# Kernel optimization log

Measured on AMD Instinct MI355X. Metric: run time of the kernel, lower is better.

## Reference

```python
import jax, jax.numpy as jnp
import numpy as np

D = 768
B = 32
N = 768


def setup_inputs() -> dict:
    key = jax.random.key(0)
    k1, k2, k3, k4 = jax.random.split(key, 4)
    stdv = 1.0 / np.sqrt(D)
    X = jax.random.normal(k1, (B, N, D), dtype=jnp.float32)
    adj = jax.random.uniform(k2, (B, N, N), dtype=jnp.float32)
    W_l = jax.random.uniform(k3, (D, D), dtype=jnp.float32, minval=-stdv, maxval=stdv)
    W_l1 = jax.random.uniform(k4, (D, D), dtype=jnp.float32, minval=-stdv, maxval=stdv)
    return {"X": X, "adj": adj, "W_l": W_l, "W_l1": W_l1}


def _row_normalize(adj):
    # rowsum^-1 with inf -> 0 (rows summing to zero stay zero)
    rowsum = adj.sum(axis=-1, keepdims=True)  # [B, N, 1]
    r_inv = jnp.where(rowsum == 0, 0.0, 1.0 / rowsum)
    return adj * r_inv


def reference(X, adj, W_l, W_l1):
    # X: [B, N, D], adj: [B, N, N]
    adj_n = _row_normalize(adj)
    e1 = jnp.einsum('bnd,de->bne', X, W_l1)        # message transform
    e11 = jnp.einsum('bnm,bmd->bnd', adj_n, e1)    # aggregate
    X1 = jnp.einsum('bnd,de->bne', X, W_l)         # self transform
    h = X1 + e11
    return jax.nn.leaky_relu(h, negative_slope=0.01)
```

## Files before the change

### kernel.cpp

```cpp
#include <hip/hip_runtime.h>
#include <hip/hip_bf16.h>
#include <cstdint>
#include <cstddef>

#define BN_ROWS 24576
#define DD 768
#define BE (768*768)
#define BM 192
#define BN_T 192
#define BK 32
#define ABUF 12288
#define BUFSZ 24576

typedef __attribute__((ext_vector_type(8))) short bf16x8;
typedef __attribute__((ext_vector_type(4))) float f32x4;
typedef __attribute__((ext_vector_type(8))) unsigned short u16x8;

static __device__ __forceinline__ unsigned short f2bf(float f) {
  unsigned int u = __builtin_bit_cast(unsigned int, f);
  unsigned int lsb = (u >> 16) & 1u;
  u += 0x7fffu + lsb;
  return (unsigned short)(u >> 16);
}

static __device__ __forceinline__ u16x8 pack8(float4 a, float4 b) {
  u16x8 o;
  o[0] = f2bf(a.x); o[1] = f2bf(a.y); o[2] = f2bf(a.z); o[3] = f2bf(a.w);
  o[4] = f2bf(b.x); o[5] = f2bf(b.y); o[6] = f2bf(b.z); o[7] = f2bf(b.w);
  return o;
}

#define CXB 2304
#define CXS (CXB * 256)

__global__ __launch_bounds__(256) void convertX(const float* __restrict__ x,
                                                unsigned short* __restrict__ xb) {
  const int u0 = blockIdx.x * 256 + threadIdx.x;
  const float4* in = reinterpret_cast<const float4*>(x);
  u16x8* outp = reinterpret_cast<u16x8*>(xb);
  float4 v[8];
  #pragma unroll
  for (int j = 0; j < 4; ++j) {
    v[2 * j]     = in[(size_t)(u0 + j * CXS) * 2];
    v[2 * j + 1] = in[(size_t)(u0 + j * CXS) * 2 + 1];
  }
  #pragma unroll
  for (int j = 0; j < 4; ++j)
    outp[u0 + j * CXS] = pack8(v[2 * j], v[2 * j + 1]);
}

#define ANB 3072

__global__ __launch_bounds__(256) void prep2(const float* __restrict__ adj,
                                             const float* __restrict__ Wl,
                                             const float* __restrict__ Wl1,
                                             unsigned short* __restrict__ adjnb,
                                             unsigned short* __restrict__ WlT,
                                             unsigned short* __restrict__ Wl1T) {
  __shared__ float tile[64][65];
  const int bid = blockIdx.x;
  if (bid < ANB) {
    const int w = threadIdx.x >> 6;
    const int hl = (threadIdx.x >> 5) & 1;
    const int l = threadIdx.x & 31;
    const int row = bid * 8 + w * 2 + hl;
    const float4* a = reinterpret_cast<const float4*>(adj + (size_t)row * DD);
    float4 v[6];
    #pragma unroll
    for (int i = 0; i < 3; ++i) {
      int u = l + i * 32;
      v[2 * i]     = a[u * 2];
      v[2 * i + 1] = a[u * 2 + 1];
    }
    float s = 0.f;
    #pragma unroll
    for (int i = 0; i < 6; ++i) s += (v[i].x + v[i].y) + (v[i].z + v[i].w);
    #pragma unroll
    for (int off = 16; off; off >>= 1) s += __shfl_xor(s, off);
    float rinv = (s == 0.f) ? 0.f : 1.f / s;
    u16x8* o = reinterpret_cast<u16x8*>(adjnb + (size_t)row * DD);
    #pragma unroll
    for (int i = 0; i < 3; ++i) {
      float4 p = v[2 * i], q = v[2 * i + 1];
      p.x *= rinv; p.y *= rinv; p.z *= rinv; p.w *= rinv;
      q.x *= rinv; q.y *= rinv; q.z *= rinv; q.w *= rinv;
      o[l + i * 32] = pack8(p, q);
    }
  } else {
    const int tb = bid - ANB;
    const int tr = tb / 12, tc = tb % 12;
    const int c = threadIdx.x & 63, r0 = threadIdx.x >> 6;
    const float* srcs[2] = {Wl, Wl1};
    unsigned short* dsts[2] = {WlT, Wl1T};
    #pragma unroll
    for (int m = 0; m < 2; ++m) {
      const float* src = srcs[m];
      #pragma unroll
      for (int i = 0; i < 16; ++i) {
        int r = r0 + i * 4;
        tile[r][c] = src[(size_t)(tr * 64 + r) * DD + tc * 64 + c];
      }
      __syncthreads();
      unsigned short* dst = dsts[m];
      #pragma unroll
      for (int i = 0; i < 16; ++i) {
        int r2 = r0 + i * 4;
        dst[(size_t)(tc * 64 + r2) * DD + tr * 64 + c] = f2bf(tile[c][r2]);
      }
      __syncthreads();
    }
  }
}


template<int MODE>
__global__ __launch_bounds__(256, 2) void gemm4(
    const unsigned short* __restrict__ P0,
    const unsigned short* __restrict__ P1,
    const unsigned short* __restrict__ P2,
    const unsigned short* __restrict__ P3,
    void* __restrict__ outp)
{
  __shared__ char smem[2 * BUFSZ];
  constexpr int NT = MODE ? 48 : 24;
  const int tid = threadIdx.x, lane = tid & 63;
  const int wid = tid >> 6;
  const int wr = wid >> 1, wc = wid & 1;

  const int logical = (blockIdx.x & 7) * 64 + (blockIdx.x >> 3);

  const unsigned short *Ab0, *Bb0, *Ab1 = nullptr, *Bb1 = nullptr;
  int mt, nt, b;
  if (MODE == 0) {
    mt = logical >> 2; nt = logical & 3;
    b = mt >> 2;
    Ab0 = P0 + (size_t)mt * BM * DD;
    Bb0 = P1 + (size_t)nt * BN_T * DD;
  } else {
    b = logical >> 4; int r = logical & 15; mt = r >> 2; nt = r & 3;
    size_t bo = (size_t)b * BE;
    Ab0 = P0 + bo + (size_t)mt * BM * DD;
    Bb0 = P1 + bo + (size_t)nt * BN_T * DD;
    Ab1 = P2 + bo + (size_t)mt * BM * DD;
    Bb1 = P3 + (size_t)nt * BN_T * DD;
  }

  const int r_in = lane >> 2;
  const int s_in = lane & 3;

  auto stage = [&](int s) {
    const int buf = (s & 1) * BUFSZ;
    const unsigned short *Ab, *Bb;
    int kk;
    if (MODE == 1 && s >= 24) { kk = s - 24; Ab = Ab1; Bb = Bb1; }
    else                      { kk = s;      Ab = Ab0; Bb = Bb0; }
    #pragma unroll
    for (int i = 0; i < 6; ++i) {
      int chunk = wid * 6 + i;
      bool isA = chunk < 12;
      int c = isA ? chunk : chunk - 12;
      int row = c * 16 + r_in;
      int slot = s_in ^ ((row >> 1) & 3);
      const unsigned short* src = (isA ? Ab : Bb) + (size_t)row * DD + kk * BK + slot * 8;
      __builtin_amdgcn_global_load_lds(
          (const __attribute__((address_space(1))) void*)src,
          (__attribute__((address_space(3))) void*)(smem + buf + (isA ? 0 : ABUF) + c * 1024),
          16, 0, 0);
    }
  };

  const int ks = lane >> 4;
  auto frag = [&](int off, int row) -> bf16x8 {
    int slot = ks ^ ((row >> 1) & 3);
    return *reinterpret_cast<const bf16x8*>(smem + off + row * 64 + slot * 16);
  };

  f32x4 acc[6][6] = {};
  const int arow = wr * 96 + (lane & 15);
  const int brow = wc * 96 + (lane & 15);

  stage(0);

  for (int t = 0; t < NT; ++t) {
    asm volatile("s_waitcnt vmcnt(0)" ::: "memory");
    __builtin_amdgcn_s_barrier();

    if (t + 1 < NT) stage(t + 1);

    const int bufA = (t & 1) * BUFSZ;
    const int bufB = bufA + ABUF;
    bf16x8 a[6], bg[6];
    #pragma unroll
    for (int i = 0; i < 6; ++i) a[i] = frag(bufA, arow + i * 16);
    #pragma unroll
    for (int i = 0; i < 6; ++i) bg[i] = frag(bufB, brow + i * 16);

    __builtin_amdgcn_s_setprio(1);
    #pragma unroll
    for (int ni = 0; ni < 6; ++ni)
      #pragma unroll
      for (int mi = 0; mi < 6; ++mi)
        acc[mi][ni] = __builtin_amdgcn_mfma_f32_16x16x32_bf16(a[mi], bg[ni], acc[mi][ni], 0, 0, 0);
    __builtin_amdgcn_s_setprio(0);
  }

  if (MODE == 0) {
    unsigned short* ob = (unsigned short*)outp + (size_t)b * BE;
    const int mloc = (mt & 3) * BM + wr * 96 + (lane >> 4) * 4;
    #pragma unroll
    for (int mi = 0; mi < 6; ++mi)
      #pragma unroll
      for (int ni = 0; ni < 6; ++ni) {
        int m = mloc + mi * 16;
        int d = nt * BN_T + wc * 96 + ni * 16 + (lane & 15);
        f32x4 v = acc[mi][ni];
        ushort4 o;
        o.x = f2bf(v[0]); o.y = f2bf(v[1]); o.z = f2bf(v[2]); o.w = f2bf(v[3]);
        *reinterpret_cast<ushort4*>(ob + (size_t)d * DD + m) = o;
      }
  } else {
    float* ob = (float*)outp + (size_t)b * BE;
    const int mloc = mt * BM + wr * 96 + (lane >> 4) * 4;
    #pragma unroll
    for (int mi = 0; mi < 6; ++mi)
      #pragma unroll
      for (int ni = 0; ni < 6; ++ni) {
        int m = mloc + mi * 16;
        int n = nt * BN_T + wc * 96 + ni * 16 + (lane & 15);
        f32x4 v = acc[mi][ni];
        #pragma unroll
        for (int j = 0; j < 4; ++j) {
          float x = v[j];
          ob[(size_t)(m + j) * DD + n] = x > 0.f ? x : 0.01f * x;
        }
      }
  }
}


extern "C" void kernel_launch(void* const* d_in, const int* in_sizes, int n_in,
                              void* d_out, int out_size, void* d_ws, size_t ws_size,
                              hipStream_t stream) {
  const float* X   = (const float*)d_in[0];
  const float* adj = (const float*)d_in[1];
  const float* Wl  = (const float*)d_in[2];
  const float* Wl1 = (const float*)d_in[3];
  float* out = (float*)d_out;

  char* ws = (char*)d_ws;
  const size_t SZ = (size_t)BN_ROWS * DD * 2;
  unsigned short* Xb    = (unsigned short*)(ws);
  unsigned short* adjnb = (unsigned short*)(ws + SZ);
  unsigned short* e1T   = (unsigned short*)(ws + 2 * SZ);
  unsigned short* WlT   = (unsigned short*)(ws + 3 * SZ);
  unsigned short* Wl1T  = (unsigned short*)(ws + 3 * SZ + (size_t)BE * 2);

  convertX<<<CXB, 256, 0, stream>>>(X, Xb);
  prep2<<<ANB + 144, 256, 0, stream>>>(adj, Wl, Wl1, adjnb, WlT, Wl1T);
  gemm4<0><<<512, 256, 0, stream>>>(Xb, Wl1T, nullptr, nullptr, e1T);
  gemm4<1><<<512, 256, 0, stream>>>(adjnb, e1T, Xb, WlT, out);
}
```

Measured before the change: 150.7 us.

## Switch GEMMs to 256x256 tiles with 8 waves and ping-pong quadrant pipelining

Replaces the 192x192, 4-wave GEMM with a 256x256, 8-wave (512-thread) kernel that uses BK=64 and a 128KB double-buffered LDS. The K step is split into four quadrant phases, and async loads of the next A/B halves are interleaved with MFMA work under fine-grained waitcnt and barriers. The grid shrinks to 288 blocks, one per CU. The aim is higher arithmetic intensity per LDS byte and better overlap of loads with MFMA, at the cost of many more barriers, heavy register pressure, and only one block per CU. 288 tiles on 256 CUs leaves a partial second wave.

```diff
diff --git a/kernel.cpp b/kernel.cpp
--- a/kernel.cpp
+++ b/kernel.cpp
@@ -6,11 +6,6 @@
 #define BN_ROWS 24576
 #define DD 768
 #define BE (768*768)
-#define BM 192
-#define BN_T 192
-#define BK 32
-#define ABUF 12288
-#define BUFSZ 24576
 
 typedef __attribute__((ext_vector_type(8))) short bf16x8;
 typedef __attribute__((ext_vector_type(4))) float f32x4;
@@ -114,105 +109,174 @@
 
 
 template<int MODE>
-__global__ __launch_bounds__(256, 2) void gemm4(
+__global__ __launch_bounds__(512) void gemm8p(
     const unsigned short* __restrict__ P0,
     const unsigned short* __restrict__ P1,
     const unsigned short* __restrict__ P2,
     const unsigned short* __restrict__ P3,
     void* __restrict__ outp)
 {
-  __shared__ char smem[2 * BUFSZ];
-  constexpr int NT = MODE ? 48 : 24;
+  __shared__ char smem[131072];
+  constexpr int NT = MODE ? 24 : 12;
   const int tid = threadIdx.x, lane = tid & 63;
   const int wid = tid >> 6;
-  const int wr = wid >> 1, wc = wid & 1;
-
-  const int logical = (blockIdx.x & 7) * 64 + (blockIdx.x >> 3);
-
-  const unsigned short *Ab0, *Bb0, *Ab1 = nullptr, *Bb1 = nullptr;
+  const int wr = wid >> 2, wc = wid & 3;
+
+  const int logical = (blockIdx.x & 7) * 36 + (blockIdx.x >> 3);
+
+  const unsigned short *Ag0, *Bg0, *Ag1 = nullptr, *Bg1 = nullptr;
   int mt, nt, b;
   if (MODE == 0) {
-    mt = logical >> 2; nt = logical & 3;
-    b = mt >> 2;
-    Ab0 = P0 + (size_t)mt * BM * DD;
-    Bb0 = P1 + (size_t)nt * BN_T * DD;
+    mt = logical / 3; nt = logical % 3;
+    b = mt / 3;
+    Ag0 = P0 + (size_t)mt * 256 * DD;
+    Bg0 = P1 + (size_t)nt * 256 * DD;
   } else {
-    b = logical >> 4; int r = logical & 15; mt = r >> 2; nt = r & 3;
+    b = logical / 9; int r = logical % 9; mt = r / 3; nt = r % 3;
     size_t bo = (size_t)b * BE;
-    Ab0 = P0 + bo + (size_t)mt * BM * DD;
-    Bb0 = P1 + bo + (size_t)nt * BN_T * DD;
-    Ab1 = P2 + bo + (size_t)mt * BM * DD;
-    Bb1 = P3 + (size_t)nt * BN_T * DD;
-  }
-
-  const int r_in = lane >> 2;
-  const int s_in = lane & 3;
-
-  auto stage = [&](int s) {
-    const int buf = (s & 1) * BUFSZ;
-    const unsigned short *Ab, *Bb;
-    int kk;
-    if (MODE == 1 && s >= 24) { kk = s - 24; Ab = Ab1; Bb = Bb1; }
-    else                      { kk = s;      Ab = Ab0; Bb = Bb0; }
-    #pragma unroll
-    for (int i = 0; i < 6; ++i) {
-      int chunk = wid * 6 + i;
-      bool isA = chunk < 12;
-      int c = isA ? chunk : chunk - 12;
-      int row = c * 16 + r_in;
-      int slot = s_in ^ ((row >> 1) & 3);
-      const unsigned short* src = (isA ? Ab : Bb) + (size_t)row * DD + kk * BK + slot * 8;
+    Ag0 = P0 + bo + (size_t)mt * 256 * DD;
+    Bg0 = P1 + bo + (size_t)nt * 256 * DD;
+    Ag1 = P2 + bo + (size_t)mt * 256 * DD;
+    Bg1 = P3 + (size_t)nt * 256 * DD;
+  }
+
+  const int srow_t = tid >> 3;
+  const int sslot = tid & 7;
+
+  auto stage = [&](int s, bool isA, int hi) {
+    int sc = s < NT ? s : 0;
+    int kk; const unsigned short* base;
+    if (MODE == 1 && sc >= 12) { kk = sc - 12; base = isA ? Ag1 : Bg1; }
+    else                       { kk = sc;      base = isA ? Ag0 : Bg0; }
+    char* region = smem + (s & 1) * 65536 + (isA ? 0 : 32768) + hi * 16384;
+    #pragma unroll
+    for (int l = 0; l < 2; ++l) {
+      int row = hi * 128 + l * 64 + srow_t;
+      const unsigned short* src = base + (size_t)row * DD + kk * 64
+                                  + (sslot ^ (row & 7)) * 8;
       __builtin_amdgcn_global_load_lds(
           (const __attribute__((address_space(1))) void*)src,
-          (__attribute__((address_space(3))) void*)(smem + buf + (isA ? 0 : ABUF) + c * 1024),
+          (__attribute__((address_space(3))) void*)(region + l * 8192 + wid * 1024),
           16, 0, 0);
     }
   };
 
   const int ks = lane >> 4;
-  auto frag = [&](int off, int row) -> bf16x8 {
-    int slot = ks ^ ((row >> 1) & 3);
-    return *reinterpret_cast<const bf16x8*>(smem + off + row * 64 + slot * 16);
+  const int l15 = lane & 15;
+  auto rdA = [&](int bufo, int rh, int fi, int kh) -> bf16x8 {
+    int row = wr * 128 + rh * 64 + fi * 16 + l15;
+    int slot = (kh * 4 + ks) ^ (row & 7);
+    return *reinterpret_cast<const bf16x8*>(smem + bufo + row * 128 + slot * 16);
   };
-
-  f32x4 acc[6][6] = {};
-  const int arow = wr * 96 + (lane & 15);
-  const int brow = wc * 96 + (lane & 15);
-
-  stage(0);
+  auto rdB = [&](int bufo, int ch, int fj, int kh) -> bf16x8 {
+    int row = wc * 64 + ch * 32 + fj * 16 + l15;
+    int slot = (kh * 4 + ks) ^ (row & 7);
+    return *reinterpret_cast<const bf16x8*>(smem + bufo + 32768 + row * 128 + slot * 16);
+  };
+
+  f32x4 acc[8][4] = {};
+  bf16x8 a0[8], a1[8], b0[4], b1[4];
+
+  stage(0, true, 0); stage(0, true, 1);
+  stage(0, false, 0); stage(0, false, 1);
+  stage(1, true, 0); stage(1, true, 1);
+  asm volatile("s_waitcnt vmcnt(4)" ::: "memory");
+  __builtin_amdgcn_s_barrier();
 
   for (int t = 0; t < NT; ++t) {
-    asm volatile("s_waitcnt vmcnt(0)" ::: "memory");
-    __builtin_amdgcn_s_barrier();
-
-    if (t + 1 < NT) stage(t + 1);
-
-    const int bufA = (t & 1) * BUFSZ;
-    const int bufB = bufA + ABUF;
-    bf16x8 a[6], bg[6];
-    #pragma unroll
-    for (int i = 0; i < 6; ++i) a[i] = frag(bufA, arow + i * 16);
-    #pragma unroll
-    for (int i = 0; i < 6; ++i) bg[i] = frag(bufB, brow + i * 16);
-
+    const int bufo = (t & 1) * 65536;
+
+    #pragma unroll
+    for (int fi = 0; fi < 4; ++fi) {
+      a0[fi * 2]     = rdA(bufo, 0, fi, 0);
+      a0[fi * 2 + 1] = rdA(bufo, 0, fi, 1);
+    }
+    #pragma unroll
+    for (int fj = 0; fj < 2; ++fj) {
+      b0[fj * 2]     = rdB(bufo, 0, fj, 0);
+      b0[fj * 2 + 1] = rdB(bufo, 0, fj, 1);
+    }
+    stage(t + 1, false, 0);
+    asm volatile("s_waitcnt vmcnt(4)" ::: "memory");
+    __builtin_amdgcn_s_barrier();
     __builtin_amdgcn_s_setprio(1);
     #pragma unroll
-    for (int ni = 0; ni < 6; ++ni)
-      #pragma unroll
-      for (int mi = 0; mi < 6; ++mi)
-        acc[mi][ni] = __builtin_amdgcn_mfma_f32_16x16x32_bf16(a[mi], bg[ni], acc[mi][ni], 0, 0, 0);
+    for (int kh = 0; kh < 2; ++kh)
+      #pragma unroll
+      for (int fi = 0; fi < 4; ++fi)
+        #pragma unroll
+        for (int fj = 0; fj < 2; ++fj)
+          acc[fi][fj] = __builtin_amdgcn_mfma_f32_16x16x32_bf16(
+              a0[fi * 2 + kh], b0[fj * 2 + kh], acc[fi][fj], 0, 0, 0);
     __builtin_amdgcn_s_setprio(0);
-  }
+    __builtin_amdgcn_s_barrier();
+
+    #pragma unroll
+    for (int fi = 0; fi < 4; ++fi) {
+      a1[fi * 2]     = rdA(bufo, 1, fi, 0);
+      a1[fi * 2 + 1] = rdA(bufo, 1, fi, 1);
+    }
+    stage(t + 1, false, 1);
+    asm volatile("s_waitcnt vmcnt(4)" ::: "memory");
+    __builtin_amdgcn_s_barrier();
+    __builtin_amdgcn_s_setprio(1);
+    #pragma unroll
+    for (int kh = 0; kh < 2; ++kh)
+      #pragma unroll
+      for (int fi = 0; fi < 4; ++fi)
+        #pragma unroll
+        for (int fj = 0; fj < 2; ++fj)
+          acc[4 + fi][fj] = __builtin_amdgcn_mfma_f32_16x16x32_bf16(
+              a1[fi * 2 + kh], b0[fj * 2 + kh], acc[4 + fi][fj], 0, 0, 0);
+    __builtin_amdgcn_s_setprio(0);
+    __builtin_amdgcn_s_barrier();
+
+    #pragma unroll
+    for (int fj = 0; fj < 2; ++fj) {
+      b1[fj * 2]     = rdB(bufo, 1, fj, 0);
+      b1[fj * 2 + 1] = rdB(bufo, 1, fj, 1);
+    }
+    stage(t + 2, true, 0);
+    asm volatile("s_waitcnt vmcnt(4)" ::: "memory");
+    __builtin_amdgcn_s_barrier();
+    __builtin_amdgcn_s_setprio(1);
+    #pragma unroll
+    for (int kh = 0; kh < 2; ++kh)
+      #pragma unroll
+      for (int fi = 0; fi < 4; ++fi)
+        #pragma unroll
+        for (int fj = 0; fj < 2; ++fj)
+          acc[4 + fi][2 + fj] = __builtin_amdgcn_mfma_f32_16x16x32_bf16(
+              a1[fi * 2 + kh], b1[fj * 2 + kh], acc[4 + fi][2 + fj], 0, 0, 0);
+    __builtin_amdgcn_s_setprio(0);
+    __builtin_amdgcn_s_barrier();
+
+    stage(t + 2, true, 1);
+    asm volatile("s_waitcnt vmcnt(4)" ::: "memory");
+    __builtin_amdgcn_s_barrier();
+    __builtin_amdgcn_s_setprio(1);
+    #pragma unroll
+    for (int kh = 0; kh < 2; ++kh)
+      #pragma unroll
+      for (int fi = 0; fi < 4; ++fi)
+        #pragma unroll
+        for (int fj = 0; fj < 2; ++fj)
+          acc[fi][2 + fj] = __builtin_amdgcn_mfma_f32_16x16x32_bf16(
+              a0[fi * 2 + kh], b1[fj * 2 + kh], acc[fi][2 + fj], 0, 0, 0);
+    __builtin_amdgcn_s_setprio(0);
+    __builtin_amdgcn_s_barrier();
+  }
+  asm volatile("s_waitcnt vmcnt(0)" ::: "memory");
 
   if (MODE == 0) {
     unsigned short* ob = (unsigned short*)outp + (size_t)b * BE;
-    const int mloc = (mt & 3) * BM + wr * 96 + (lane >> 4) * 4;
-    #pragma unroll
-    for (int mi = 0; mi < 6; ++mi)
-      #pragma unroll
-      for (int ni = 0; ni < 6; ++ni) {
+    const int mloc = (mt % 3) * 256 + wr * 128 + (lane >> 4) * 4;
+    #pragma unroll
+    for (int mi = 0; mi < 8; ++mi)
+      #pragma unroll
+      for (int ni = 0; ni < 4; ++ni) {
         int m = mloc + mi * 16;
-        int d = nt * BN_T + wc * 96 + ni * 16 + (lane & 15);
+        int d = nt * 256 + wc * 64 + ni * 16 + l15;
         f32x4 v = acc[mi][ni];
         ushort4 o;
         o.x = f2bf(v[0]); o.y = f2bf(v[1]); o.z = f2bf(v[2]); o.w = f2bf(v[3]);
@@ -220,13 +284,13 @@
       }
   } else {
     float* ob = (float*)outp + (size_t)b * BE;
-    const int mloc = mt * BM + wr * 96 + (lane >> 4) * 4;
-    #pragma unroll
-    for (int mi = 0; mi < 6; ++mi)
-      #pragma unroll
-      for (int ni = 0; ni < 6; ++ni) {
+    const int mloc = mt * 256 + wr * 128 + (lane >> 4) * 4;
+    #pragma unroll
+    for (int mi = 0; mi < 8; ++mi)
+      #pragma unroll
+      for (int ni = 0; ni < 4; ++ni) {
         int m = mloc + mi * 16;
-        int n = nt * BN_T + wc * 96 + ni * 16 + (lane & 15);
+        int n = nt * 256 + wc * 64 + ni * 16 + l15;
         f32x4 v = acc[mi][ni];
         #pragma unroll
         for (int j = 0; j < 4; ++j) {
@@ -257,6 +321,6 @@
 
   convertX<<<CXB, 256, 0, stream>>>(X, Xb);
   prep2<<<ANB + 144, 256, 0, stream>>>(adj, Wl, Wl1, adjnb, WlT, Wl1T);
-  gemm4<0><<<512, 256, 0, stream>>>(Xb, Wl1T, nullptr, nullptr, e1T);
-  gemm4<1><<<512, 256, 0, stream>>>(adjnb, e1T, Xb, WlT, out);
-}
+  gemm8p<0><<<288, 512, 0, stream>>>(Xb, Wl1T, nullptr, nullptr, e1T);
+  gemm8p<1><<<288, 512, 0, stream>>>(adjnb, e1T, Xb, WlT, out);
+}
```

After: 195.5 us. 1.3x slower.
